# Optimization experiments

Hardware: AMD Instinct MI355X
Metric: run time of the kernel (lower is better)

Reference implementation:

```python
import jax, jax.numpy as jnp
import numpy as np
from jax import lax


def _make_kernel(k, factor):
    k = jnp.asarray(k, dtype=jnp.float32)
    if k.ndim == 1:
        k = k[None, :] * k[:, None]
    k = k / jnp.sum(k)
    return k * (factor ** 2)


def setup_inputs() -> dict:
    key = jax.random.key(0)
    x = jax.random.normal(key, (8, 64, 256, 256), dtype=jnp.float32)
    factor = 2
    kernel = _make_kernel([1.0, 3.0, 3.0, 1.0], factor)  # (4, 4), sums to factor^2
    return {"x": x, "kernel": kernel, "factor": factor}


def _upfirdn2d(x, kernel, up, down, pad0, pad1):
    # x: (N, C, H, W); kernel: (kh, kw)
    N, C, H, W = x.shape
    kh, kw = kernel.shape
    # torch does conv2d (cross-correlation) with the flipped kernel -> true convolution.
    w = jnp.flip(kernel, (0, 1))[None, None].astype(x.dtype)  # (1, 1, kh, kw)
    xr = x.reshape(N * C, 1, H, W)
    # lhs_dilation inserts up-1 zeros BETWEEN samples; the native torch code also
    # appends up-1 trailing zeros per row/col (H*up total), so add (up-1) to the
    # trailing pad to reproduce the exact same padded extent.
    pads = ((pad0, pad1 + up - 1), (pad0, pad1 + up - 1))
    out = lax.conv_general_dilated(
        xr, w,
        window_strides=(1, 1),
        padding=pads,
        lhs_dilation=(up, up),
        dimension_numbers=("NCHW", "OIHW", "NCHW"),
    )
    out = out[:, :, ::down, ::down]
    return out.reshape(N, C, out.shape[-2], out.shape[-1])


def reference(x, kernel, factor):
    kh = kernel.shape[0]
    p = kh - factor
    pad0 = (p + 1) // 2 + factor - 1
    pad1 = p // 2
    return _upfirdn2d(x, kernel, up=factor, down=1, pad0=pad0, pad1=pad1)
```

## Files before the change

### kernel.cpp

```cpp
#include <hip/hip_runtime.h>
#include <stdint.h>


#define IN_H 256
#define IN_W 256
#define OUT_H 512
#define OUT_W 512

__global__ __launch_bounds__(256) void upfirdn2x_kernel(
    const float* __restrict__ x,
    const float* __restrict__ k2,
    float* __restrict__ out)
{
    const int t  = threadIdx.x & 63;
    const int ty = threadIdx.x >> 6;
    const int y  = blockIdx.x * 4 + ty;
    const int ch = blockIdx.y;

    const int py = y & 1;
    const int i  = y >> 1;

    int rA, rB, krA, krB;
    if (py == 0) { rA = i - 1; krA = 3; rB = i;     krB = 1; }
    else         { rA = i;     krA = 2; rB = i + 1; krB = 0; }
    const bool vA = (rA >= 0) && (rA < IN_H);
    const bool vB = (rB >= 0) && (rB < IN_H);
    const int rAc = vA ? rA : 0;
    const int rBc = vB ? rB : 0;

    float wA[4], wB[4];
#pragma unroll
    for (int c = 0; c < 4; ++c) {
        wA[c] = vA ? k2[krA * 4 + c] : 0.0f;
        wB[c] = vB ? k2[krB * 4 + c] : 0.0f;
    }

    const float* xc   = x + (size_t)ch * (IN_H * IN_W);
    const float* rowA = xc + rAc * IN_W;
    const float* rowB = xc + rBc * IN_W;

    const int c0 = 4 * t;
    const float4 a4 = *reinterpret_cast<const float4*>(rowA + c0);
    const float4 b4 = *reinterpret_cast<const float4*>(rowB + c0);

    float cA[6], cB[6];
    cA[0] = (t > 0)  ? rowA[c0 - 1] : 0.0f;
    cB[0] = (t > 0)  ? rowB[c0 - 1] : 0.0f;
    cA[5] = (t < 63) ? rowA[c0 + 4] : 0.0f;
    cB[5] = (t < 63) ? rowB[c0 + 4] : 0.0f;
    cA[1] = a4.x; cA[2] = a4.y; cA[3] = a4.z; cA[4] = a4.w;
    cB[1] = b4.x; cB[2] = b4.y; cB[3] = b4.z; cB[4] = b4.w;

    float o[8];
#pragma unroll
    for (int u = 0; u < 8; ++u) {
        const int u2 = u >> 1;
        if ((u & 1) == 0) {
            o[u] = wA[3] * cA[u2] + wA[1] * cA[u2 + 1]
                 + wB[3] * cB[u2] + wB[1] * cB[u2 + 1];
        } else {
            o[u] = wA[2] * cA[u2 + 1] + wA[0] * cA[u2 + 2]
                 + wB[2] * cB[u2 + 1] + wB[0] * cB[u2 + 2];
        }
    }

    float* op = out + (size_t)ch * (OUT_H * OUT_W) + (size_t)y * OUT_W + 8 * t;
    *reinterpret_cast<float4*>(op)     = make_float4(o[0], o[1], o[2], o[3]);
    *reinterpret_cast<float4*>(op + 4) = make_float4(o[4], o[5], o[6], o[7]);
}

extern "C" void kernel_launch(void* const* d_in, const int* in_sizes, int n_in,
                              void* d_out, int out_size, void* d_ws, size_t ws_size,
                              hipStream_t stream) {
    const float* x  = (const float*)d_in[0];
    const float* k2 = (const float*)d_in[1];
    float* out = (float*)d_out;

    const int nch = in_sizes[0] / (IN_H * IN_W);
    dim3 block(256);
    dim3 grid(OUT_H / 4, nch);
    upfirdn2x_kernel<<<grid, block, 0, stream>>>(x, k2, out);
}
```

Baseline: 679.9 us.

## Compute two output rows per input row pair and use nontemporal stores

Each thread now loads one pair of adjacent input rows and produces both output rows that depend on them (rows 2q+1 and 2q+2), instead of one output row per thread. This halves the number of input row loads and roughly halves the thread count. Output writes switch to nontemporal stores to avoid polluting the cache with streaming output. Edge pairs handle boundary validity by zeroing the missing row and skipping the invalid store.

```diff
diff --git a/kernel.cpp b/kernel.cpp
--- a/kernel.cpp
+++ b/kernel.cpp
@@ -7,6 +7,8 @@
 #define OUT_H 512
 #define OUT_W 512
 
+typedef float f4 __attribute__((ext_vector_type(4)));
+
 __global__ __launch_bounds__(256) void upfirdn2x_kernel(
     const float* __restrict__ x,
     const float* __restrict__ k2,
@@ -14,34 +16,20 @@
 {
     const int t  = threadIdx.x & 63;
     const int ty = threadIdx.x >> 6;
-    const int y  = blockIdx.x * 4 + ty;
+    const int q  = blockIdx.x * 4 + ty - 1;
+    if (q >= IN_H) return;
     const int ch = blockIdx.y;
 
-    const int py = y & 1;
-    const int i  = y >> 1;
-
-    int rA, rB, krA, krB;
-    if (py == 0) { rA = i - 1; krA = 3; rB = i;     krB = 1; }
-    else         { rA = i;     krA = 2; rB = i + 1; krB = 0; }
-    const bool vA = (rA >= 0) && (rA < IN_H);
-    const bool vB = (rB >= 0) && (rB < IN_H);
-    const int rAc = vA ? rA : 0;
-    const int rBc = vB ? rB : 0;
-
-    float wA[4], wB[4];
-#pragma unroll
-    for (int c = 0; c < 4; ++c) {
-        wA[c] = vA ? k2[krA * 4 + c] : 0.0f;
-        wB[c] = vB ? k2[krB * 4 + c] : 0.0f;
-    }
+    const bool vA = (q >= 0);
+    const bool vB = (q + 1 < IN_H);
 
     const float* xc   = x + (size_t)ch * (IN_H * IN_W);
-    const float* rowA = xc + rAc * IN_W;
-    const float* rowB = xc + rBc * IN_W;
+    const float* rowA = xc + (size_t)(vA ? q     : 0) * IN_W;
+    const float* rowB = xc + (size_t)(vB ? q + 1 : 0) * IN_W;
 
     const int c0 = 4 * t;
-    const float4 a4 = *reinterpret_cast<const float4*>(rowA + c0);
-    const float4 b4 = *reinterpret_cast<const float4*>(rowB + c0);
+    const f4 a4 = *reinterpret_cast<const f4*>(rowA + c0);
+    const f4 b4 = *reinterpret_cast<const f4*>(rowB + c0);
 
     float cA[6], cB[6];
     cA[0] = (t > 0)  ? rowA[c0 - 1] : 0.0f;
@@ -51,22 +39,47 @@
     cA[1] = a4.x; cA[2] = a4.y; cA[3] = a4.z; cA[4] = a4.w;
     cB[1] = b4.x; cB[2] = b4.y; cB[3] = b4.z; cB[4] = b4.w;
 
-    float o[8];
+    if (!vA) {
+#pragma unroll
+        for (int c = 0; c < 6; ++c) cA[c] = 0.0f;
+    }
+    if (!vB) {
+#pragma unroll
+        for (int c = 0; c < 6; ++c) cB[c] = 0.0f;
+    }
+
+    float kw[16];
+#pragma unroll
+    for (int i = 0; i < 16; ++i) kw[i] = k2[i];
+
+    float o1[8], o2[8];
 #pragma unroll
     for (int u = 0; u < 8; ++u) {
-        const int u2 = u >> 1;
+        const int j = u >> 1;
         if ((u & 1) == 0) {
-            o[u] = wA[3] * cA[u2] + wA[1] * cA[u2 + 1]
-                 + wB[3] * cB[u2] + wB[1] * cB[u2 + 1];
+            o1[u] = kw[8+3]*cA[j]  + kw[8+1]*cA[j+1]  + kw[0+3]*cB[j]  + kw[0+1]*cB[j+1];
+            o2[u] = kw[12+3]*cA[j] + kw[12+1]*cA[j+1] + kw[4+3]*cB[j]  + kw[4+1]*cB[j+1];
         } else {
-            o[u] = wA[2] * cA[u2 + 1] + wA[0] * cA[u2 + 2]
-                 + wB[2] * cB[u2 + 1] + wB[0] * cB[u2 + 2];
+            o1[u] = kw[8+2]*cA[j+1]  + kw[8+0]*cA[j+2]  + kw[0+2]*cB[j+1] + kw[0+0]*cB[j+2];
+            o2[u] = kw[12+2]*cA[j+1] + kw[12+0]*cA[j+2] + kw[4+2]*cB[j+1] + kw[4+0]*cB[j+2];
         }
     }
 
-    float* op = out + (size_t)ch * (OUT_H * OUT_W) + (size_t)y * OUT_W + 8 * t;
-    *reinterpret_cast<float4*>(op)     = make_float4(o[0], o[1], o[2], o[3]);
-    *reinterpret_cast<float4*>(op + 4) = make_float4(o[4], o[5], o[6], o[7]);
+    float* ob = out + (size_t)ch * (OUT_H * OUT_W);
+    if (vA) {
+        float* op = ob + (size_t)(2 * q + 1) * OUT_W + 8 * t;
+        f4 s0; s0.x = o1[0]; s0.y = o1[1]; s0.z = o1[2]; s0.w = o1[3];
+        f4 s1; s1.x = o1[4]; s1.y = o1[5]; s1.z = o1[6]; s1.w = o1[7];
+        __builtin_nontemporal_store(s0, reinterpret_cast<f4*>(op));
+        __builtin_nontemporal_store(s1, reinterpret_cast<f4*>(op + 4));
+    }
+    if (vB) {
+        float* op = ob + (size_t)(2 * q + 2) * OUT_W + 8 * t;
+        f4 s0; s0.x = o2[0]; s0.y = o2[1]; s0.z = o2[2]; s0.w = o2[3];
+        f4 s1; s1.x = o2[4]; s1.y = o2[5]; s1.z = o2[6]; s1.w = o2[7];
+        __builtin_nontemporal_store(s0, reinterpret_cast<f4*>(op));
+        __builtin_nontemporal_store(s1, reinterpret_cast<f4*>(op + 4));
+    }
 }
 
 extern "C" void kernel_launch(void* const* d_in, const int* in_sizes, int n_in,
@@ -77,7 +90,8 @@
     float* out = (float*)d_out;
 
     const int nch = in_sizes[0] / (IN_H * IN_W);
+    const int npairs = IN_H + 1;
     dim3 block(256);
-    dim3 grid(OUT_H / 4, nch);
+    dim3 grid((npairs + 3) / 4, nch);
     upfirdn2x_kernel<<<grid, block, 0, stream>>>(x, k2, out);
 }
```

Measured after the change: 616.3 us. -9.3%, faster.
